# Kernel optimization log

Measured on AMD Instinct MI355X. Metric: run time of the kernel, lower is better.

## Reference

```python
import jax, jax.numpy as jnp
import numpy as np

BLOCK_SIZE = 32
BITS = 4
Q_MAX = 2 ** (BITS - 1) - 1  # 7


def setup_inputs() -> dict:
    key = jax.random.key(0)
    k1, k2, k3, k4 = jax.random.split(key, 4)
    B, S, D_in, D_out = 4, 2048, 4096, 4096
    x = jax.random.normal(k1, (B, S, D_in), dtype=jnp.float32)
    # 4-bit symmetric quantized values in [-8, 7], stored as int32
    weight_q = jax.random.randint(k2, (D_out, D_in), -(2 ** (BITS - 1)), 2 ** (BITS - 1), dtype=jnp.int32)
    # per-block positive scales (abs-max of each block in the original)
    block_scales = jax.random.uniform(k3, (D_out, D_in // BLOCK_SIZE), dtype=jnp.float32, minval=0.01, maxval=1.0)
    bias = jax.random.normal(k4, (D_out,), dtype=jnp.float32) * 0.01
    return {"x": x, "weight_q": weight_q, "block_scales": block_scales, "bias": bias}


def _dequantize(weight_q, block_scales):
    out_f, in_f = weight_q.shape
    n_blocks = in_f // BLOCK_SIZE
    q = weight_q.reshape(out_f, n_blocks, BLOCK_SIZE).astype(jnp.float32)
    w = q / Q_MAX * block_scales[:, :, None]
    return w.reshape(out_f, in_f)


def reference(x, weight_q, block_scales, bias):
    # block dequantize: w = q / q_max * scale, then y = x @ w.T + b
    w = _dequantize(weight_q, block_scales)  # [out, in] fp32
    return jnp.einsum('bsi,oi->bso', x, w) + bias
```

## Files before the change

### kernel.cpp

```cpp
#include <hip/hip_runtime.h>
#include <stdint.h>

#define M_DIM 8192
#define N_DIM 4096
#define K_DIM 4096
#define NBLK  (K_DIM / 32)

typedef __attribute__((ext_vector_type(4))) float          f32x4;
typedef __attribute__((ext_vector_type(8))) short          bf16x8;
typedef __attribute__((ext_vector_type(4))) int            i32x4;
typedef __attribute__((ext_vector_type(8))) unsigned short u16x8;
typedef __attribute__((address_space(3))) unsigned short   lds_us;

__device__ __forceinline__ unsigned short f2bf(float f) {
  unsigned u = __builtin_bit_cast(unsigned, f);
  u += 0x7fffu + ((u >> 16) & 1u);
  return (unsigned short)(u >> 16);
}

__device__ __forceinline__ void stage16(const unsigned short* g, lds_us* l) {
  __builtin_amdgcn_global_load_lds(
      (const __attribute__((address_space(1))) void*)g,
      (__attribute__((address_space(3))) void*)l, 16, 0, 0);
}

template <int OFF>
__device__ __forceinline__ bf16x8 dsr(lds_us* addr) {
  bf16x8 d;
  asm volatile("ds_read_b128 %0, %1 offset:%2" : "=v"(d) : "v"(addr), "n"(OFF));
  return d;
}

__global__ void MXFP4_dequant_kernel(const int* __restrict__ wq,
                                     const float* __restrict__ scales,
                                     unsigned short* __restrict__ wb) {
  int t = blockIdx.x * 256 + threadIdx.x;
  long e = (long)t * 8;
  int o = t >> 9;
  int k = (t & 511) << 3;
  float s = scales[o * NBLK + (k >> 5)] * (1.0f / 7.0f);
  i32x4 q0 = *(const i32x4*)(wq + e);
  i32x4 q1 = *(const i32x4*)(wq + e + 4);
  u16x8 r;
#pragma unroll
  for (int j = 0; j < 4; ++j) r[j]     = f2bf((float)q0[j] * s);
#pragma unroll
  for (int j = 0; j < 4; ++j) r[4 + j] = f2bf((float)q1[j] * s);
  *(u16x8*)(wb + e) = r;
}

__global__ void MXFP4_cvt_kernel(const float* __restrict__ x,
                                 unsigned short* __restrict__ xb) {
  long t = (long)blockIdx.x * 256 + threadIdx.x;
  long e = t * 8;
  f32x4 v0 = *(const f32x4*)(x + e);
  f32x4 v1 = *(const f32x4*)(x + e + 4);
  u16x8 r;
#pragma unroll
  for (int j = 0; j < 4; ++j) r[j]     = f2bf(v0[j]);
#pragma unroll
  for (int j = 0; j < 4; ++j) r[4 + j] = f2bf(v1[j]);
  *(u16x8*)(xb + e) = r;
}


#define BAR() __builtin_amdgcn_s_barrier()
#define WAIT_LGKM0() do { asm volatile("s_waitcnt lgkmcnt(0)" ::: "memory"); \
                          __builtin_amdgcn_sched_barrier(0); } while (0)

#define ST_A(t_, h_, BUFA_, valid_) do { \
  if (valid_) { \
    const unsigned short* s_ = srcA + (size_t)(h_) * 128 * K_DIM + (t_) * 64; \
    lds_us* d_ = lp + (BUFA_) * 16384 + ((h_) * 8 + wv) * 1024; \
    stage16(s_, d_); stage16(s_ + 32, d_ + 512); \
  } else { stage16(srcA, lp + 65536); stage16(srcA + 32, lp + 65536 + 512); } \
} while (0)

#define ST_B(t_, h_, BUFB_, valid_) do { \
  if (valid_) { \
    const unsigned short* s_ = srcB + (size_t)(h_) * 128 * K_DIM + (t_) * 64; \
    lds_us* d_ = lp + 32768 + (BUFB_) * 16384 + ((h_) * 8 + wv) * 1024; \
    stage16(s_, d_); stage16(s_ + 32, d_ + 512); \
  } else { stage16(srcB, lp + 65536); stage16(srcB + 32, lp + 65536 + 512); } \
} while (0)

#define MF(MB_, NB_, AF_, BF_) do { \
  _Pragma("unroll") \
  for (int kk_ = 0; kk_ < 2; ++kk_) \
    _Pragma("unroll") \
    for (int mm_ = 0; mm_ < 4; ++mm_) \
      _Pragma("unroll") \
      for (int nn_ = 0; nn_ < 2; ++nn_) \
        acc[(MB_) + mm_][(NB_) + nn_] = __builtin_amdgcn_mfma_f32_16x16x32_bf16( \
            AF_[mm_][kk_], BF_[nn_][kk_], acc[(MB_) + mm_][(NB_) + nn_], 0, 0, 0); \
} while (0)

#define GROUP(BUF_, tB_, tA_, vB_, vA_) do { \
  lds_us* dsA_ = lp + (BUF_) * 16384 + wm * 8192 + lane * 8; \
  lds_us* dsB_ = lp + 32768 + (BUF_) * 16384 + wn * 4096 + lane * 8; \
   \
  aLo[0][0] = dsr<0>(dsA_);      aLo[0][1] = dsr<1024>(dsA_); \
  aLo[1][0] = dsr<2048>(dsA_);   aLo[1][1] = dsr<3072>(dsA_); \
  aLo[2][0] = dsr<4096>(dsA_);   aLo[2][1] = dsr<5120>(dsA_); \
  aLo[3][0] = dsr<6144>(dsA_);   aLo[3][1] = dsr<7168>(dsA_); \
  bLo[0][0] = dsr<0>(dsB_);      bLo[0][1] = dsr<1024>(dsB_); \
  bLo[1][0] = dsr<2048>(dsB_);   bLo[1][1] = dsr<3072>(dsB_); \
  ST_B(tB_, 0, (BUF_) ^ 1, vB_); \
  BAR(); WAIT_LGKM0(); \
  __builtin_amdgcn_s_setprio(1); \
  MF(0, 0, aLo, bLo); \
  __builtin_amdgcn_s_setprio(0); \
  BAR(); \
   \
  aHi[0][0] = dsr<8192>(dsA_);   aHi[0][1] = dsr<9216>(dsA_); \
  aHi[1][0] = dsr<10240>(dsA_);  aHi[1][1] = dsr<11264>(dsA_); \
  aHi[2][0] = dsr<12288>(dsA_);  aHi[2][1] = dsr<13312>(dsA_); \
  aHi[3][0] = dsr<14336>(dsA_);  aHi[3][1] = dsr<15360>(dsA_); \
  ST_B(tB_, 1, (BUF_) ^ 1, vB_); \
  BAR(); WAIT_LGKM0(); \
  __builtin_amdgcn_s_setprio(1); \
  MF(4, 0, aHi, bLo); \
  __builtin_amdgcn_s_setprio(0); \
  BAR(); \
   \
  bHi[0][0] = dsr<4096>(dsB_);   bHi[0][1] = dsr<5120>(dsB_); \
  bHi[1][0] = dsr<6144>(dsB_);   bHi[1][1] = dsr<7168>(dsB_); \
  ST_A(tA_, 0, (BUF_), vA_); \
  BAR(); WAIT_LGKM0(); \
  __builtin_amdgcn_s_setprio(1); \
  MF(0, 2, aLo, bHi); \
  __builtin_amdgcn_s_setprio(0); \
  BAR(); \
   \
  ST_A(tA_, 1, (BUF_), vA_); \
  asm volatile("s_waitcnt vmcnt(4)" ::: "memory"); \
  BAR(); \
  __builtin_amdgcn_s_setprio(1); \
  MF(4, 2, aHi, bHi); \
  __builtin_amdgcn_s_setprio(0); \
  BAR(); \
} while (0)

__global__ __launch_bounds__(512, 2) void MXFP4_gemm_kernel(
    const unsigned short* __restrict__ A,
    const unsigned short* __restrict__ B,
    const float* __restrict__ bias,
    float* __restrict__ C) {
  __shared__ unsigned short LDS[66560];
  lds_us* lp = (lds_us*)LDS;

  const int tid  = threadIdx.x;
  const int lane = tid & 63;
  const int wv   = tid >> 6;
  const int wm   = wv >> 2;
  const int wn   = wv & 3;

  const int bid = blockIdx.x;
  const int sw  = (bid & 7) * 64 + (bid >> 3);
  const int tn  = sw >> 5;
  const int tm  = sw & 31;
  const int brow = tm * 256;
  const int bcol = tn * 256;

  const unsigned short* srcA =
      A + (size_t)(brow + wv * 16 + (lane & 15)) * K_DIM + ((lane >> 4) * 8);
  const unsigned short* srcB =
      B + (size_t)(bcol + wv * 16 + (lane & 15)) * K_DIM + ((lane >> 4) * 8);

  f32x4 acc[8][4] = {};
  bf16x8 aLo[4][2], aHi[4][2], bLo[2][2], bHi[2][2];

  ST_A(0, 0, 0, true); ST_A(0, 1, 0, true);
  ST_B(0, 0, 0, true); ST_B(0, 1, 0, true);
  ST_A(1, 0, 1, true); ST_A(1, 1, 1, true);
  asm volatile("s_waitcnt vmcnt(4)" ::: "memory");
  BAR();

  for (int it = 0; it < 31; ++it) {
    const int g0 = 2 * it;
    GROUP(0, g0 + 1, g0 + 2, true, true);
    GROUP(1, g0 + 2, g0 + 3, true, true);
  }
  GROUP(0, 63, 64, true, false);
  GROUP(1, 64, 65, false, false);

  const int rb = brow + wm * 128 + (lane >> 4) * 4;
  const int cb = bcol + wn * 64 + (lane & 15);
#pragma unroll
  for (int n = 0; n < 4; ++n) {
    const int col = cb + n * 16;
    const float bv = bias[col];
#pragma unroll
    for (int m = 0; m < 8; ++m) {
      const int row = rb + m * 16;
#pragma unroll
      for (int j = 0; j < 4; ++j)
        C[(size_t)(row + j) * N_DIM + col] = acc[m][n][j] + bv;
    }
  }
}

extern "C" void kernel_launch(void* const* d_in, const int* in_sizes, int n_in,
                              void* d_out, int out_size, void* d_ws, size_t ws_size,
                              hipStream_t stream) {
  const float* x      = (const float*)d_in[0];
  const int*   wq     = (const int*)d_in[1];
  const float* scales = (const float*)d_in[2];
  const float* bias   = (const float*)d_in[3];
  float*       out    = (float*)d_out;

  unsigned short* wb = (unsigned short*)d_ws;
  unsigned short* xb = wb + (size_t)N_DIM * K_DIM;

  MXFP4_dequant_kernel<<<(N_DIM * (long)K_DIM / 8) / 256, 256, 0, stream>>>(wq, scales, wb);
  MXFP4_cvt_kernel<<<(M_DIM * (long)K_DIM / 8) / 256, 256, 0, stream>>>(x, xb);

  MXFP4_gemm_kernel<<<512, 512, 0, stream>>>(xb, wb, bias, out);
}
```

Baseline: 327.7 us.

## Pre-tile bf16 operands in LDS order for contiguous global-to-LDS loads

```diff
diff --git a/kernel.cpp b/kernel.cpp
--- a/kernel.cpp
+++ b/kernel.cpp
@@ -31,36 +31,51 @@
   return d;
 }
 
+
 __global__ void MXFP4_dequant_kernel(const int* __restrict__ wq,
                                      const float* __restrict__ scales,
                                      unsigned short* __restrict__ wb) {
-  int t = blockIdx.x * 256 + threadIdx.x;
-  long e = (long)t * 8;
-  int o = t >> 9;
-  int k = (t & 511) << 3;
-  float s = scales[o * NBLK + (k >> 5)] * (1.0f / 7.0f);
-  i32x4 q0 = *(const i32x4*)(wq + e);
-  i32x4 q1 = *(const i32x4*)(wq + e + 4);
-  u16x8 r;
-#pragma unroll
-  for (int j = 0; j < 4; ++j) r[j]     = f2bf((float)q0[j] * s);
-#pragma unroll
-  for (int j = 0; j < 4; ++j) r[4 + j] = f2bf((float)q1[j] * s);
-  *(u16x8*)(wb + e) = r;
+  size_t t = (size_t)blockIdx.x * 256 + threadIdx.x;
+  int slot = (int)(t & 63);
+  int r = slot & 15, c = slot >> 4;
+  int sub = (int)(t >> 6) & 15;
+  int R = sub >> 1, Kt = sub & 1;
+  int H = (int)(t >> 10) & 31;
+  int g = (int)(t >> 15);
+  size_t row = (size_t)H * 128 + R * 16 + r;
+  size_t k   = (size_t)g * 64 + Kt * 32 + c * 8;
+  float s = scales[row * NBLK + (g * 2 + Kt)] * (1.0f / 7.0f);
+  const int* src = wq + row * K_DIM + k;
+  i32x4 q0 = *(const i32x4*)src;
+  i32x4 q1 = *(const i32x4*)(src + 4);
+  u16x8 out;
+#pragma unroll
+  for (int j = 0; j < 4; ++j) out[j]     = f2bf((float)q0[j] * s);
+#pragma unroll
+  for (int j = 0; j < 4; ++j) out[4 + j] = f2bf((float)q1[j] * s);
+  *(u16x8*)(wb + t * 8) = out;
 }
 
 __global__ void MXFP4_cvt_kernel(const float* __restrict__ x,
                                  unsigned short* __restrict__ xb) {
-  long t = (long)blockIdx.x * 256 + threadIdx.x;
-  long e = t * 8;
-  f32x4 v0 = *(const f32x4*)(x + e);
-  f32x4 v1 = *(const f32x4*)(x + e + 4);
-  u16x8 r;
-#pragma unroll
-  for (int j = 0; j < 4; ++j) r[j]     = f2bf(v0[j]);
-#pragma unroll
-  for (int j = 0; j < 4; ++j) r[4 + j] = f2bf(v1[j]);
-  *(u16x8*)(xb + e) = r;
+  size_t t = (size_t)blockIdx.x * 256 + threadIdx.x;
+  int slot = (int)(t & 63);
+  int r = slot & 15, c = slot >> 4;
+  int sub = (int)(t >> 6) & 15;
+  int R = sub >> 1, Kt = sub & 1;
+  int H = (int)(t >> 10) & 63;
+  int g = (int)(t >> 16);
+  size_t row = (size_t)H * 128 + R * 16 + r;
+  size_t k   = (size_t)g * 64 + Kt * 32 + c * 8;
+  const float* src = x + row * K_DIM + k;
+  f32x4 v0 = *(const f32x4*)src;
+  f32x4 v1 = *(const f32x4*)(src + 4);
+  u16x8 out;
+#pragma unroll
+  for (int j = 0; j < 4; ++j) out[j]     = f2bf(v0[j]);
+#pragma unroll
+  for (int j = 0; j < 4; ++j) out[4 + j] = f2bf(v1[j]);
+  *(u16x8*)(xb + t * 8) = out;
 }
 
 
@@ -70,18 +85,20 @@
 
 #define ST_A(t_, h_, BUFA_, valid_) do { \
   if (valid_) { \
-    const unsigned short* s_ = srcA + (size_t)(h_) * 128 * K_DIM + (t_) * 64; \
-    lds_us* d_ = lp + (BUFA_) * 16384 + ((h_) * 8 + wv) * 1024; \
-    stage16(s_, d_); stage16(s_ + 32, d_ + 512); \
-  } else { stage16(srcA, lp + 65536); stage16(srcA + 32, lp + 65536 + 512); } \
+    const unsigned short* s_ = Abase + ((size_t)(t_) * 64 + (h_)) * 8192 + tid8; \
+    lds_us* d_ = lp + (BUFA_) * 16384 + (h_) * 8192 + tid8; \
+    stage16(s_, d_); stage16(s_ + 4096, d_ + 4096); \
+  } else { stage16(Abase + tid8, lp + 65536); \
+           stage16(Abase + tid8 + 4096, lp + 65536 + 512); } \
 } while (0)
 
 #define ST_B(t_, h_, BUFB_, valid_) do { \
   if (valid_) { \
-    const unsigned short* s_ = srcB + (size_t)(h_) * 128 * K_DIM + (t_) * 64; \
-    lds_us* d_ = lp + 32768 + (BUFB_) * 16384 + ((h_) * 8 + wv) * 1024; \
-    stage16(s_, d_); stage16(s_ + 32, d_ + 512); \
-  } else { stage16(srcB, lp + 65536); stage16(srcB + 32, lp + 65536 + 512); } \
+    const unsigned short* s_ = Bbase + ((size_t)(t_) * 32 + (h_)) * 8192 + tid8; \
+    lds_us* d_ = lp + 32768 + (BUFB_) * 16384 + (h_) * 8192 + tid8; \
+    stage16(s_, d_); stage16(s_ + 4096, d_ + 4096); \
+  } else { stage16(Bbase + tid8, lp + 65536); \
+           stage16(Bbase + tid8 + 4096, lp + 65536 + 512); } \
 } while (0)
 
 #define MF(MB_, NB_, AF_, BF_) do { \
@@ -154,18 +171,18 @@
   const int wv   = tid >> 6;
   const int wm   = wv >> 2;
   const int wn   = wv & 3;
+  const int tid8 = tid * 8;
 
   const int bid = blockIdx.x;
-  const int sw  = (bid & 7) * 64 + (bid >> 3);
-  const int tn  = sw >> 5;
-  const int tm  = sw & 31;
+  const int xcd = bid & 7;
+  const int idx = bid >> 3;
+  const int tm  = (xcd & 3) * 8 + (idx & 7);
+  const int tn  = (xcd >> 2) * 8 + (idx >> 3);
   const int brow = tm * 256;
   const int bcol = tn * 256;
 
-  const unsigned short* srcA =
-      A + (size_t)(brow + wv * 16 + (lane & 15)) * K_DIM + ((lane >> 4) * 8);
-  const unsigned short* srcB =
-      B + (size_t)(bcol + wv * 16 + (lane & 15)) * K_DIM + ((lane >> 4) * 8);
+  const unsigned short* Abase = A + (size_t)(tm * 2) * 8192;
+  const unsigned short* Bbase = B + (size_t)(tn * 2) * 8192;
 
   f32x4 acc[8][4] = {};
   bf16x8 aLo[4][2], aHi[4][2], bLo[2][2], bHi[2][2];
```

After: 303.7 us. -7.3%, faster.
